# Kernel tuning notes

Hardware: AMD Instinct MI355X
Metric: run time of the kernel (lower is better)

Reference implementation:

```python
import jax, jax.numpy as jnp
import numpy as np

N = 2048
D_MODEL = 1024
N_HEADS = 16
D_HEAD = D_MODEL // N_HEADS


def setup_inputs() -> dict:
    key = jax.random.key(0)
    ks = jax.random.split(key, 12)
    s = 1.0 / np.sqrt(D_MODEL)
    inp = {
        "x": jax.random.normal(ks[0], (N, D_MODEL), dtype=jnp.float32),
        "edge_bias": jax.random.normal(ks[1], (N, N, N_HEADS), dtype=jnp.float32) * 0.1,
        # torch.nn.Linear convention: y = x @ W.T + b, W: [out, in]
        "Wq": jax.random.normal(ks[2], (D_MODEL, D_MODEL), dtype=jnp.float32) * s,
        "bq": jax.random.normal(ks[3], (D_MODEL,), dtype=jnp.float32) * s,
        "Wk": jax.random.normal(ks[4], (D_MODEL, D_MODEL), dtype=jnp.float32) * s,
        "bk": jax.random.normal(ks[5], (D_MODEL,), dtype=jnp.float32) * s,
        "Wv": jax.random.normal(ks[6], (D_MODEL, D_MODEL), dtype=jnp.float32) * s,
        "bv": jax.random.normal(ks[7], (D_MODEL,), dtype=jnp.float32) * s,
        "Wo": jax.random.normal(ks[8], (D_MODEL, D_MODEL), dtype=jnp.float32) * s,
        "bo": jax.random.normal(ks[9], (D_MODEL,), dtype=jnp.float32) * s,
    }
    return inp


def reference(x, edge_bias, Wq, bq, Wk, bk, Wv, bv, Wo, bo):
    # x: [N, d], edge_bias: [N, N, H]
    scale = D_HEAD ** -0.5
    q = (x @ Wq.T + bq).reshape(N, N_HEADS, D_HEAD)  # [N, H, Dh]
    k = (x @ Wk.T + bk).reshape(N, N_HEADS, D_HEAD)
    v = (x @ Wv.T + bv).reshape(N, N_HEADS, D_HEAD)
    # attn[h, i, j] = q_i . k_j * scale + edge_bias[i, j, h]
    attn = jnp.einsum("nhd,mhd->hnm", q, k) * scale
    attn = attn + jnp.transpose(edge_bias, (2, 0, 1))
    attn = jax.nn.softmax(attn, axis=-1)
    # dropout is identity in eval/reference mode
    out = jnp.einsum("hnm,mhd->nhd", attn, v).reshape(N, D_MODEL)
    return out @ Wo.T + bo
```

## Files before the change

### kernel.cpp

```cpp
#include <hip/hip_runtime.h>
#include <math.h>

#define NTOK 2048
#define DM   1024
#define NH   16
#define DH   64
#define GM   2048
#define GN   1024
#define GK   1024
#define SCALE 0.125f

typedef __attribute__((ext_vector_type(8))) short short8;
typedef __attribute__((ext_vector_type(4))) float floatx4;
typedef unsigned short ushort_t;

__device__ __forceinline__ unsigned short f2bf(float f) {
    unsigned u = __builtin_bit_cast(unsigned, f);
    u += 0x7fffu + ((u >> 16) & 1u);
    return (unsigned short)(u >> 16);
}

__global__ __launch_bounds__(256) void convert5(
    const float* __restrict__ x,  const float* __restrict__ wq,
    const float* __restrict__ wk, const float* __restrict__ wv,
    const float* __restrict__ wo, ushort_t* __restrict__ dst)
{
    const size_t i4 = (size_t)blockIdx.x * 256 + threadIdx.x;
    const float* src; size_t off;
    if      (i4 <  524288) { src = x;  off = 0;       }
    else if (i4 <  786432) { src = wq; off = 524288;  }
    else if (i4 < 1048576) { src = wk; off = 786432;  }
    else if (i4 < 1310720) { src = wv; off = 1048576; }
    else                   { src = wo; off = 1310720; }
    float4 v = ((const float4*)src)[i4 - off];
    ushort4 o;
    o.x = f2bf(v.x); o.y = f2bf(v.y); o.z = f2bf(v.z); o.w = f2bf(v.w);
    ((ushort4*)dst)[i4] = o;
}

template<int BM, int BN>
__global__ __launch_bounds__(256) void gemm_bt(
    const ushort_t* __restrict__ A,
    const ushort_t* __restrict__ B0, const ushort_t* __restrict__ B1,
    const ushort_t* __restrict__ B2,
    const float* __restrict__ bi0, const float* __restrict__ bi1,
    const float* __restrict__ bi2,
    void* C0, void* C1, void* C2, int mode0, int mode1, int mode2)
{
    constexpr int AC = BM * 4 / 256;
    constexpr int BC = BN * 4 / 256;
    constexpr int FI = BM / 32;
    constexpr int FJ = BN / 32;
    constexpr int WM = BM / 2;
    constexpr int WN = BN / 2;

    const int z = blockIdx.z;
    const ushort_t* B   = (z == 0) ? B0  : (z == 1) ? B1  : B2;
    const float*    bia = (z == 0) ? bi0 : (z == 1) ? bi1 : bi2;
    void*           C   = (z == 0) ? C0  : (z == 1) ? C1  : C2;
    const int mode      = (z == 0) ? mode0 : (z == 1) ? mode1 : mode2;

    __shared__ __align__(16) ushort_t As[BM][32];
    __shared__ __align__(16) ushort_t Bs[BN][32];

    const int t    = threadIdx.x;
    const int w    = t >> 6;
    const int L    = t & 63;
    const int r16  = L & 15;
    const int quad = L >> 4;
    const int wm   = w & 1;
    const int wn   = w >> 1;

    const int m0 = blockIdx.y * BM;
    const int n0 = blockIdx.x * BN;

    const int srow = t >> 2;
    const int skc  = (t & 3) * 8;

    const ushort_t* ap = A + (size_t)(m0 + srow) * GK + skc;
    const ushort_t* bp = B + (size_t)(n0 + srow) * GK + skc;

    floatx4 acc[FI][FJ];
#pragma unroll
    for (int i = 0; i < FI; ++i)
#pragma unroll
        for (int j = 0; j < FJ; ++j) acc[i][j] = (floatx4){0.f, 0.f, 0.f, 0.f};

    short8 areg[AC], breg[BC];
#pragma unroll
    for (int c = 0; c < AC; ++c) areg[c] = *(const short8*)(ap + (size_t)c * 64 * GK);
#pragma unroll
    for (int c = 0; c < BC; ++c) breg[c] = *(const short8*)(bp + (size_t)c * 64 * GK);

    for (int ks = 0; ks < GK / 32; ++ks) {
        __syncthreads();
#pragma unroll
        for (int c = 0; c < AC; ++c) *(short8*)&As[c * 64 + srow][skc] = areg[c];
#pragma unroll
        for (int c = 0; c < BC; ++c) *(short8*)&Bs[c * 64 + srow][skc] = breg[c];
        __syncthreads();
        if (ks < GK / 32 - 1) {
            ap += 32; bp += 32;
#pragma unroll
            for (int c = 0; c < AC; ++c) areg[c] = *(const short8*)(ap + (size_t)c * 64 * GK);
#pragma unroll
            for (int c = 0; c < BC; ++c) breg[c] = *(const short8*)(bp + (size_t)c * 64 * GK);
        }
        short8 af[FI], bf[FJ];
#pragma unroll
        for (int fi = 0; fi < FI; ++fi)
            af[fi] = *(const short8*)&As[wm * WM + fi * 16 + r16][quad * 8];
#pragma unroll
        for (int fj = 0; fj < FJ; ++fj)
            bf[fj] = *(const short8*)&Bs[wn * WN + fj * 16 + r16][quad * 8];
#pragma unroll
        for (int fi = 0; fi < FI; ++fi)
#pragma unroll
            for (int fj = 0; fj < FJ; ++fj)
                acc[fi][fj] = __builtin_amdgcn_mfma_f32_16x16x32_bf16(
                    af[fi], bf[fj], acc[fi][fj], 0, 0, 0);
    }

#pragma unroll
    for (int fj = 0; fj < FJ; ++fj) {
        const int col = n0 + wn * WN + fj * 16 + r16;
        const float bv = bia[col];
#pragma unroll
        for (int fi = 0; fi < FI; ++fi) {
            const int row0 = m0 + wm * WM + fi * 16 + 4 * quad;
            floatx4 c = acc[fi][fj];
            if (mode == 2) {
                float* Cf = (float*)C;
#pragma unroll
                for (int i = 0; i < 4; ++i)
                    Cf[(size_t)(row0 + i) * GN + col] = c[i] + bv;
            } else if (mode == 0) {
                ushort_t* Cb = (ushort_t*)C;
#pragma unroll
                for (int i = 0; i < 4; ++i)
                    Cb[(size_t)(row0 + i) * GN + col] = f2bf(c[i] + bv);
            } else {
                ushort_t* Cb = (ushort_t*)C;
                ushort4 pk;
                pk.x = f2bf(c[0] + bv); pk.y = f2bf(c[1] + bv);
                pk.z = f2bf(c[2] + bv); pk.w = f2bf(c[3] + bv);
                *(ushort4*)(Cb + (size_t)col * GM + row0) = pk;
            }
        }
    }
}

#define NT   (NTOK / 32)
#define NCH  4
#define NTCH (NT / NCH)
#define JCH  (NTOK / NCH)

__global__ __launch_bounds__(256) void attn2(
    const ushort_t* __restrict__ q, const ushort_t* __restrict__ k,
    const ushort_t* __restrict__ vT, const float* __restrict__ bias,
    float* __restrict__ opart, float* __restrict__ lpart)
{
    __shared__ float    Bb[2][4][16][33];
    __shared__ ushort_t Ps[4][16][40];

    const int b    = blockIdx.x;
    const int ch   = blockIdx.y;
    const int jb   = ch * JCH;
    const int hg   = (b >> 3) & 3;
    const int it   = (b & 7) | ((b >> 5) << 3);
    const int i0   = it * 16;
    const int t    = threadIdx.x;
    const int w    = t >> 6;
    const int L    = t & 63;
    const int r16  = L & 15;
    const int quad = L >> 4;
    const int h    = hg * 4 + w;

#define kAddr(J0, JH, KC) (k  + (size_t)((J0) + (JH)*16 + r16) * DM + h*DH + (KC)*32 + quad*8)
#define vAddr(J0, DB)     (vT + (size_t)(h*DH + (DB)*16 + r16) * NTOK + (J0) + quad*8)
#define bAddr(J0, CI)     (bias + ((size_t)(i0 + (CI)*8 + (t>>5)) * NTOK + (J0) + (t&31)) * NH + hg*4)

    short8 qf[2];
#pragma unroll
    for (int kc = 0; kc < 2; ++kc)
        qf[kc] = *(const short8*)(q + (size_t)(i0 + r16) * DM + h * DH + kc * 32 + quad * 8);

    short8 kf[2][4];
    short8 vf[2][4];
    float4 bst[2];

    kf[0][0] = *(const short8*)kAddr(jb, 0, 0);
    kf[0][1] = *(const short8*)kAddr(jb, 0, 1);
    kf[0][2] = *(const short8*)kAddr(jb, 1, 0);
    kf[0][3] = *(const short8*)kAddr(jb, 1, 1);
    vf[0][0] = *(const short8*)vAddr(jb, 0);
    vf[0][1] = *(const short8*)vAddr(jb, 1);
    vf[0][2] = *(const short8*)vAddr(jb, 2);
    vf[0][3] = *(const short8*)vAddr(jb, 3);
    bst[0] = *(const float4*)bAddr(jb, 0);
    bst[1] = *(const float4*)bAddr(jb, 1);
    Bb[0][0][0 + (t >> 5)][t & 31] = bst[0].x;
    Bb[0][1][0 + (t >> 5)][t & 31] = bst[0].y;
    Bb[0][2][0 + (t >> 5)][t & 31] = bst[0].z;
    Bb[0][3][0 + (t >> 5)][t & 31] = bst[0].w;
    Bb[0][0][8 + (t >> 5)][t & 31] = bst[1].x;
    Bb[0][1][8 + (t >> 5)][t & 31] = bst[1].y;
    Bb[0][2][8 + (t >> 5)][t & 31] = bst[1].z;
    Bb[0][3][8 + (t >> 5)][t & 31] = bst[1].w;
    __syncthreads();

    floatx4 o[4];
#pragma unroll
    for (int d = 0; d < 4; ++d) o[d] = (floatx4){0.f, 0.f, 0.f, 0.f};
    float lrow[4] = {0.f, 0.f, 0.f, 0.f};

#define TILE(JT, CUR, NXT)                                                      \
  {                                                                             \
    const bool pre = (JT) < NTCH - 1;                                           \
    const int j0n = jb + ((JT) + 1) * 32;                                       \
    if (pre) {                                                                  \
      kf[NXT][0] = *(const short8*)kAddr(j0n, 0, 0);                            \
      kf[NXT][1] = *(const short8*)kAddr(j0n, 0, 1);                            \
      kf[NXT][2] = *(const short8*)kAddr(j0n, 1, 0);                            \
      kf[NXT][3] = *(const short8*)kAddr(j0n, 1, 1);                            \
      vf[NXT][0] = *(const short8*)vAddr(j0n, 0);                               \
      vf[NXT][1] = *(const short8*)vAddr(j0n, 1);                               \
      vf[NXT][2] = *(const short8*)vAddr(j0n, 2);                               \
      vf[NXT][3] = *(const short8*)vAddr(j0n, 3);                               \
      bst[0] = *(const float4*)bAddr(j0n, 0);                                   \
      bst[1] = *(const float4*)bAddr(j0n, 1);                                   \
    }                                                                           \
    floatx4 s0 = (floatx4){0.f, 0.f, 0.f, 0.f};                                 \
    floatx4 s1 = (floatx4){0.f, 0.f, 0.f, 0.f};                                 \
    s0 = __builtin_amdgcn_mfma_f32_16x16x32_bf16(qf[0], kf[CUR][0], s0, 0,0,0); \
    s0 = __builtin_amdgcn_mfma_f32_16x16x32_bf16(qf[1], kf[CUR][1], s0, 0,0,0); \
    s1 = __builtin_amdgcn_mfma_f32_16x16x32_bf16(qf[0], kf[CUR][2], s1, 0,0,0); \
    s1 = __builtin_amdgcn_mfma_f32_16x16x32_bf16(qf[1], kf[CUR][3], s1, 0,0,0); \
    _Pragma("unroll")                                                           \
    for (int ii = 0; ii < 4; ++ii) {                                            \
      const float bv0 = Bb[CUR][w][4 * quad + ii][r16];                         \
      const float bv1 = Bb[CUR][w][4 * quad + ii][16 + r16];                    \
      const float p0 = __expf(fmaf(s0[ii], SCALE, bv0));                        \
      const float p1 = __expf(fmaf(s1[ii], SCALE, bv1));                        \
      lrow[ii] += p0 + p1;                                                      \
      Ps[w][4 * quad + ii][r16]      = f2bf(p0);                                \
      Ps[w][4 * quad + ii][16 + r16] = f2bf(p1);                                \
    }                                                                           \
    short8 pf = *(const short8*)&Ps[w][r16][quad * 8];                          \
    o[0] = __builtin_amdgcn_mfma_f32_16x16x32_bf16(pf, vf[CUR][0], o[0], 0,0,0);\
    o[1] = __builtin_amdgcn_mfma_f32_16x16x32_bf16(pf, vf[CUR][1], o[1], 0,0,0);\
    o[2] = __builtin_amdgcn_mfma_f32_16x16x32_bf16(pf, vf[CUR][2], o[2], 0,0,0);\
    o[3] = __builtin_amdgcn_mfma_f32_16x16x32_bf16(pf, vf[CUR][3], o[3], 0,0,0);\
    if (pre) {                                                                  \
      Bb[NXT][0][0 + (t >> 5)][t & 31] = bst[0].x;                              \
      Bb[NXT][1][0 + (t >> 5)][t & 31] = bst[0].y;                              \
      Bb[NXT][2][0 + (t >> 5)][t & 31] = bst[0].z;                              \
      Bb[NXT][3][0 + (t >> 5)][t & 31] = bst[0].w;                              \
      Bb[NXT][0][8 + (t >> 5)][t & 31] = bst[1].x;                              \
      Bb[NXT][1][8 + (t >> 5)][t & 31] = bst[1].y;                              \
      Bb[NXT][2][8 + (t >> 5)][t & 31] = bst[1].z;                              \
      Bb[NXT][3][8 + (t >> 5)][t & 31] = bst[1].w;                              \
    }                                                                           \
    __syncthreads();                                                            \
  }

    for (int jt = 0; jt < NTCH; jt += 2) {
        TILE(jt, 0, 1)
        TILE(jt + 1, 1, 0)
    }

    float lred[4];
#pragma unroll
    for (int ii = 0; ii < 4; ++ii) {
        float s = lrow[ii];
#pragma unroll
        for (int d = 1; d < 16; d <<= 1) s += __shfl_xor(s, d);
        lred[ii] = s;
    }
    if (r16 == 0) {
#pragma unroll
        for (int ii = 0; ii < 4; ++ii)
            lpart[(size_t)ch * NH * NTOK + (size_t)h * NTOK + i0 + 4 * quad + ii] = lred[ii];
    }

    float* op = opart + (size_t)ch * NTOK * DM;
#pragma unroll
    for (int db = 0; db < 4; ++db)
#pragma unroll
        for (int ii = 0; ii < 4; ++ii)
            op[(size_t)(i0 + 4 * quad + ii) * DM + h * DH + db * 16 + r16] = o[db][ii];
#undef TILE
#undef kAddr
#undef vAddr
#undef bAddr
}

__global__ __launch_bounds__(256) void attn_fin(
    const float* __restrict__ opart, const float* __restrict__ lpart,
    ushort_t* __restrict__ ao)
{
    const int idx = blockIdx.x * 256 + threadIdx.x;
    const int n   = idx >> 8;
    const int d4  = idx & 255;
    const int h   = d4 >> 4;
    const size_t base = (size_t)n * DM + (size_t)d4 * 4;
    float4 s = {0.f, 0.f, 0.f, 0.f};
    float  l = 0.f;
#pragma unroll
    for (int c = 0; c < NCH; ++c) {
        float4 p = *(const float4*)(opart + (size_t)c * NTOK * DM + base);
        s.x += p.x; s.y += p.y; s.z += p.z; s.w += p.w;
        l += lpart[(size_t)c * NH * NTOK + (size_t)h * NTOK + n];
    }
    const float inv = 1.f / l;
    ushort4 o;
    o.x = f2bf(s.x * inv); o.y = f2bf(s.y * inv);
    o.z = f2bf(s.z * inv); o.w = f2bf(s.w * inv);
    ((ushort4*)ao)[idx] = o;
}

extern "C" void kernel_launch(void* const* d_in, const int* in_sizes, int n_in,
                              void* d_out, int out_size, void* d_ws, size_t ws_size,
                              hipStream_t stream)
{
    const float* x  = (const float*)d_in[0];
    const float* eb = (const float*)d_in[1];
    const float* Wq = (const float*)d_in[2];
    const float* bq = (const float*)d_in[3];
    const float* Wk = (const float*)d_in[4];
    const float* bk = (const float*)d_in[5];
    const float* Wv = (const float*)d_in[6];
    const float* bv = (const float*)d_in[7];
    const float* Wo = (const float*)d_in[8];
    const float* bo = (const float*)d_in[9];
    float* out = (float*)d_out;
    (void)in_sizes; (void)n_in; (void)out_size; (void)ws_size;

    const size_t E1 = (size_t)1024 * 1024;
    ushort_t* wsb = (ushort_t*)d_ws;
    ushort_t* xb  = wsb;
    ushort_t* Wqb = wsb + 2 * E1;
    ushort_t* Wkb = wsb + 3 * E1;
    ushort_t* Wvb = wsb + 4 * E1;
    ushort_t* Wob = wsb + 5 * E1;
    ushort_t* qb  = wsb + 6 * E1;
    ushort_t* kb  = wsb + 8 * E1;
    ushort_t* vTb = wsb + 10 * E1;
    ushort_t* aob = wsb + 12 * E1;
    float* opart = (float*)(wsb + 14 * E1);
    float* lpart = opart + (size_t)NCH * NTOK * DM;

    convert5<<<6144, 256, 0, stream>>>(x, Wq, Wk, Wv, Wo, wsb);

    {
        dim3 grid(GN / 64, GM / 128, 3);
        gemm_bt<128, 64><<<grid, 256, 0, stream>>>(
            xb, Wqb, Wkb, Wvb, bq, bk, bv,
            qb, kb, vTb, 0, 0, 1);
    }
    {
        dim3 grid(512, NCH, 1);
        attn2<<<grid, 256, 0, stream>>>(qb, kb, vTb, eb, opart, lpart);
    }
    attn_fin<<<NTOK * DM / 4 / 256, 256, 0, stream>>>(opart, lpart, aob);

    {
        dim3 grid(GN / 64, GM / 64, 1);
        gemm_bt<64, 64><<<grid, 256, 0, stream>>>(
            aob, Wob, Wob, Wob, bo, bo, bo,
            out, out, out, 2, 2, 2);
    }
}
```

Measured before the change: 528.9 us.

## Process all heads per attention block to coalesce edge-bias loads

```diff
diff --git a/kernel.cpp b/kernel.cpp
--- a/kernel.cpp
+++ b/kernel.cpp
@@ -155,30 +155,32 @@
 #define NTCH (NT / NCH)
 #define JCH  (NTOK / NCH)
 
-__global__ __launch_bounds__(256) void attn2(
+__global__ __launch_bounds__(1024) void attn3(
     const ushort_t* __restrict__ q, const ushort_t* __restrict__ k,
     const ushort_t* __restrict__ vT, const float* __restrict__ bias,
     float* __restrict__ opart, float* __restrict__ lpart)
 {
-    __shared__ float    Bb[2][4][16][33];
-    __shared__ ushort_t Ps[4][16][40];
-
-    const int b    = blockIdx.x;
+    __shared__ float    Bb[2][16][16][33];
+    __shared__ ushort_t Ps[16][16][40];
+
+    const int it   = blockIdx.x;
     const int ch   = blockIdx.y;
     const int jb   = ch * JCH;
-    const int hg   = (b >> 3) & 3;
-    const int it   = (b & 7) | ((b >> 5) << 3);
     const int i0   = it * 16;
     const int t    = threadIdx.x;
     const int w    = t >> 6;
     const int L    = t & 63;
     const int r16  = L & 15;
     const int quad = L >> 4;
-    const int h    = hg * 4 + w;
+    const int h    = w;
+
+    const int si = t >> 6;
+    const int sj = (L >> 1);
+    const int sh = (L & 1) * 8;
 
 #define kAddr(J0, JH, KC) (k  + (size_t)((J0) + (JH)*16 + r16) * DM + h*DH + (KC)*32 + quad*8)
 #define vAddr(J0, DB)     (vT + (size_t)(h*DH + (DB)*16 + r16) * NTOK + (J0) + quad*8)
-#define bAddr(J0, CI)     (bias + ((size_t)(i0 + (CI)*8 + (t>>5)) * NTOK + (J0) + (t&31)) * NH + hg*4)
+#define bAddr(J0)         (bias + ((size_t)(i0 + si) * NTOK + (J0) + sj) * NH + sh)
 
     short8 qf[2];
 #pragma unroll
@@ -197,16 +199,16 @@
     vf[0][1] = *(const short8*)vAddr(jb, 1);
     vf[0][2] = *(const short8*)vAddr(jb, 2);
     vf[0][3] = *(const short8*)vAddr(jb, 3);
-    bst[0] = *(const float4*)bAddr(jb, 0);
-    bst[1] = *(const float4*)bAddr(jb, 1);
-    Bb[0][0][0 + (t >> 5)][t & 31] = bst[0].x;
-    Bb[0][1][0 + (t >> 5)][t & 31] = bst[0].y;
-    Bb[0][2][0 + (t >> 5)][t & 31] = bst[0].z;
-    Bb[0][3][0 + (t >> 5)][t & 31] = bst[0].w;
-    Bb[0][0][8 + (t >> 5)][t & 31] = bst[1].x;
-    Bb[0][1][8 + (t >> 5)][t & 31] = bst[1].y;
-    Bb[0][2][8 + (t >> 5)][t & 31] = bst[1].z;
-    Bb[0][3][8 + (t >> 5)][t & 31] = bst[1].w;
+    bst[0] = *(const float4*)bAddr(jb);
+    bst[1] = *(const float4*)(bAddr(jb) + 4);
+    Bb[0][sh + 0][si][sj] = bst[0].x;
+    Bb[0][sh + 1][si][sj] = bst[0].y;
+    Bb[0][sh + 2][si][sj] = bst[0].z;
+    Bb[0][sh + 3][si][sj] = bst[0].w;
+    Bb[0][sh + 4][si][sj] = bst[1].x;
+    Bb[0][sh + 5][si][sj] = bst[1].y;
+    Bb[0][sh + 6][si][sj] = bst[1].z;
+    Bb[0][sh + 7][si][sj] = bst[1].w;
     __syncthreads();
 
     floatx4 o[4];
@@ -227,8 +229,8 @@
       vf[NXT][1] = *(const short8*)vAddr(j0n, 1);                               \
       vf[NXT][2] = *(const short8*)vAddr(j0n, 2);                               \
       vf[NXT][3] = *(const short8*)vAddr(j0n, 3);                               \
-      bst[0] = *(const float4*)bAddr(j0n, 0);                                   \
-      bst[1] = *(const float4*)bAddr(j0n, 1);                                   \
+      bst[0] = *(const float4*)bAddr(j0n);                                      \
+      bst[1] = *(const float4*)(bAddr(j0n) + 4);                                \
     }                                                                           \
     floatx4 s0 = (floatx4){0.f, 0.f, 0.f, 0.f};                                 \
     floatx4 s1 = (floatx4){0.f, 0.f, 0.f, 0.f};                                 \
@@ -252,14 +254,14 @@
     o[2] = __builtin_amdgcn_mfma_f32_16x16x32_bf16(pf, vf[CUR][2], o[2], 0,0,0);\
     o[3] = __builtin_amdgcn_mfma_f32_16x16x32_bf16(pf, vf[CUR][3], o[3], 0,0,0);\
     if (pre) {                                                                  \
-      Bb[NXT][0][0 + (t >> 5)][t & 31] = bst[0].x;                              \
-      Bb[NXT][1][0 + (t >> 5)][t & 31] = bst[0].y;                              \
-      Bb[NXT][2][0 + (t >> 5)][t & 31] = bst[0].z;                              \
-      Bb[NXT][3][0 + (t >> 5)][t & 31] = bst[0].w;                              \
-      Bb[NXT][0][8 + (t >> 5)][t & 31] = bst[1].x;                              \
-      Bb[NXT][1][8 + (t >> 5)][t & 31] = bst[1].y;                              \
-      Bb[NXT][2][8 + (t >> 5)][t & 31] = bst[1].z;                              \
-      Bb[NXT][3][8 + (t >> 5)][t & 31] = bst[1].w;                              \
+      Bb[NXT][sh + 0][si][sj] = bst[0].x;                                       \
+      Bb[NXT][sh + 1][si][sj] = bst[0].y;                                       \
+      Bb[NXT][sh + 2][si][sj] = bst[0].z;                                       \
+      Bb[NXT][sh + 3][si][sj] = bst[0].w;                                       \
+      Bb[NXT][sh + 4][si][sj] = bst[1].x;                                       \
+      Bb[NXT][sh + 5][si][sj] = bst[1].y;                                       \
+      Bb[NXT][sh + 6][si][sj] = bst[1].z;                                       \
+      Bb[NXT][sh + 7][si][sj] = bst[1].w;                                       \
     }                                                                           \
     __syncthreads();                                                            \
   }
@@ -359,8 +361,8 @@
             qb, kb, vTb, 0, 0, 1);
     }
     {
-        dim3 grid(512, NCH, 1);
-        attn2<<<grid, 256, 0, stream>>>(qb, kb, vTb, eb, opart, lpart);
+        dim3 grid(NTOK / 16, NCH, 1);
+        attn3<<<grid, 1024, 0, stream>>>(qb, kb, vTb, eb, opart, lpart);
     }
     attn_fin<<<NTOK * DM / 4 / 256, 256, 0, stream>>>(opart, lpart, aob);
 
```

New measurement: 560.4 us. 6.0% more time.

## Process 32 query rows per attention block to reuse K/V fragments

Applied to the files above, without the earlier changes.

```diff
diff --git a/kernel.cpp b/kernel.cpp
--- a/kernel.cpp
+++ b/kernel.cpp
@@ -154,13 +154,14 @@
 #define NCH  4
 #define NTCH (NT / NCH)
 #define JCH  (NTOK / NCH)
-
-__global__ __launch_bounds__(256) void attn2(
+#define IB   32
+
+__global__ __launch_bounds__(256) void attn4(
     const ushort_t* __restrict__ q, const ushort_t* __restrict__ k,
     const ushort_t* __restrict__ vT, const float* __restrict__ bias,
     float* __restrict__ opart, float* __restrict__ lpart)
 {
-    __shared__ float    Bb[2][4][16][33];
+    __shared__ float    Bb[2][4][IB][33];
     __shared__ ushort_t Ps[4][16][40];
 
     const int b    = blockIdx.x;
@@ -168,7 +169,7 @@
     const int jb   = ch * JCH;
     const int hg   = (b >> 3) & 3;
     const int it   = (b & 7) | ((b >> 5) << 3);
-    const int i0   = it * 16;
+    const int i0   = it * IB;
     const int t    = threadIdx.x;
     const int w    = t >> 6;
     const int L    = t & 63;
@@ -180,15 +181,22 @@
 #define vAddr(J0, DB)     (vT + (size_t)(h*DH + (DB)*16 + r16) * NTOK + (J0) + quad*8)
 #define bAddr(J0, CI)     (bias + ((size_t)(i0 + (CI)*8 + (t>>5)) * NTOK + (J0) + (t&31)) * NH + hg*4)
 
-    short8 qf[2];
-#pragma unroll
-    for (int kc = 0; kc < 2; ++kc)
-        qf[kc] = *(const short8*)(q + (size_t)(i0 + r16) * DM + h * DH + kc * 32 + quad * 8);
+    short8 qf[2][2];
+#pragma unroll
+    for (int r = 0; r < 2; ++r)
+#pragma unroll
+        for (int kc = 0; kc < 2; ++kc)
+            qf[r][kc] = *(const short8*)(q + (size_t)(i0 + r * 16 + r16) * DM
+                                           + h * DH + kc * 32 + quad * 8);
 
     short8 kf[2][4];
     short8 vf[2][4];
-    float4 bst[2];
-
+    float4 bst[4];
+
+    bst[0] = *(const float4*)bAddr(jb, 0);
+    bst[1] = *(const float4*)bAddr(jb, 1);
+    bst[2] = *(const float4*)bAddr(jb, 2);
+    bst[3] = *(const float4*)bAddr(jb, 3);
     kf[0][0] = *(const short8*)kAddr(jb, 0, 0);
     kf[0][1] = *(const short8*)kAddr(jb, 0, 1);
     kf[0][2] = *(const short8*)kAddr(jb, 1, 0);
@@ -197,28 +205,31 @@
     vf[0][1] = *(const short8*)vAddr(jb, 1);
     vf[0][2] = *(const short8*)vAddr(jb, 2);
     vf[0][3] = *(const short8*)vAddr(jb, 3);
-    bst[0] = *(const float4*)bAddr(jb, 0);
-    bst[1] = *(const float4*)bAddr(jb, 1);
-    Bb[0][0][0 + (t >> 5)][t & 31] = bst[0].x;
-    Bb[0][1][0 + (t >> 5)][t & 31] = bst[0].y;
-    Bb[0][2][0 + (t >> 5)][t & 31] = bst[0].z;
-    Bb[0][3][0 + (t >> 5)][t & 31] = bst[0].w;
-    Bb[0][0][8 + (t >> 5)][t & 31] = bst[1].x;
-    Bb[0][1][8 + (t >> 5)][t & 31] = bst[1].y;
-    Bb[0][2][8 + (t >> 5)][t & 31] = bst[1].z;
-    Bb[0][3][8 + (t >> 5)][t & 31] = bst[1].w;
+#pragma unroll
+    for (int ci = 0; ci < 4; ++ci) {
+        Bb[0][0][ci * 8 + (t >> 5)][t & 31] = bst[ci].x;
+        Bb[0][1][ci * 8 + (t >> 5)][t & 31] = bst[ci].y;
+        Bb[0][2][ci * 8 + (t >> 5)][t & 31] = bst[ci].z;
+        Bb[0][3][ci * 8 + (t >> 5)][t & 31] = bst[ci].w;
+    }
     __syncthreads();
 
-    floatx4 o[4];
-#pragma unroll
-    for (int d = 0; d < 4; ++d) o[d] = (floatx4){0.f, 0.f, 0.f, 0.f};
-    float lrow[4] = {0.f, 0.f, 0.f, 0.f};
+    floatx4 o[2][4];
+#pragma unroll
+    for (int r = 0; r < 2; ++r)
+#pragma unroll
+        for (int d = 0; d < 4; ++d) o[r][d] = (floatx4){0.f, 0.f, 0.f, 0.f};
+    float lrow[2][4] = {{0.f,0.f,0.f,0.f},{0.f,0.f,0.f,0.f}};
 
 #define TILE(JT, CUR, NXT)                                                      \
   {                                                                             \
     const bool pre = (JT) < NTCH - 1;                                           \
     const int j0n = jb + ((JT) + 1) * 32;                                       \
     if (pre) {                                                                  \
+      bst[0] = *(const float4*)bAddr(j0n, 0);                                   \
+      bst[1] = *(const float4*)bAddr(j0n, 1);                                   \
+      bst[2] = *(const float4*)bAddr(j0n, 2);                                   \
+      bst[3] = *(const float4*)bAddr(j0n, 3);                                   \
       kf[NXT][0] = *(const short8*)kAddr(j0n, 0, 0);                            \
       kf[NXT][1] = *(const short8*)kAddr(j0n, 0, 1);                            \
       kf[NXT][2] = *(const short8*)kAddr(j0n, 1, 0);                            \
@@ -227,39 +238,61 @@
       vf[NXT][1] = *(const short8*)vAddr(j0n, 1);                               \
       vf[NXT][2] = *(const short8*)vAddr(j0n, 2);                               \
       vf[NXT][3] = *(const short8*)vAddr(j0n, 3);                               \
-      bst[0] = *(const float4*)bAddr(j0n, 0);                                   \
-      bst[1] = *(const float4*)bAddr(j0n, 1);                                   \
-    }                                                                           \
-    floatx4 s0 = (floatx4){0.f, 0.f, 0.f, 0.f};                                 \
-    floatx4 s1 = (floatx4){0.f, 0.f, 0.f, 0.f};                                 \
-    s0 = __builtin_amdgcn_mfma_f32_16x16x32_bf16(qf[0], kf[CUR][0], s0, 0,0,0); \
-    s0 = __builtin_amdgcn_mfma_f32_16x16x32_bf16(qf[1], kf[CUR][1], s0, 0,0,0); \
-    s1 = __builtin_amdgcn_mfma_f32_16x16x32_bf16(qf[0], kf[CUR][2], s1, 0,0,0); \
-    s1 = __builtin_amdgcn_mfma_f32_16x16x32_bf16(qf[1], kf[CUR][3], s1, 0,0,0); \
+    }                                                                           \
+    floatx4 s00 = (floatx4){0.f,0.f,0.f,0.f};                                   \
+    floatx4 s01 = (floatx4){0.f,0.f,0.f,0.f};                                   \
+    floatx4 s10 = (floatx4){0.f,0.f,0.f,0.f};                                   \
+    floatx4 s11 = (floatx4){0.f,0.f,0.f,0.f};                                   \
+    s00 = __builtin_amdgcn_mfma_f32_16x16x32_bf16(qf[0][0], kf[CUR][0], s00, 0,0,0); \
+    s00 = __builtin_amdgcn_mfma_f32_16x16x32_bf16(qf[0][1], kf[CUR][1], s00, 0,0,0); \
+    s01 = __builtin_amdgcn_mfma_f32_16x16x32_bf16(qf[0][0], kf[CUR][2], s01, 0,0,0); \
+    s01 = __builtin_amdgcn_mfma_f32_16x16x32_bf16(qf[0][1], kf[CUR][3], s01, 0,0,0); \
+    s10 = __builtin_amdgcn_mfma_f32_16x16x32_bf16(qf[1][0], kf[CUR][0], s10, 0,0,0); \
+    s10 = __builtin_amdgcn_mfma_f32_16x16x32_bf16(qf[1][1], kf[CUR][1], s10, 0,0,0); \
+    s11 = __builtin_amdgcn_mfma_f32_16x16x32_bf16(qf[1][0], kf[CUR][2], s11, 0,0,0); \
+    s11 = __builtin_amdgcn_mfma_f32_16x16x32_bf16(qf[1][1], kf[CUR][3], s11, 0,0,0); \
     _Pragma("unroll")                                                           \
     for (int ii = 0; ii < 4; ++ii) {                                            \
       const float bv0 = Bb[CUR][w][4 * quad + ii][r16];                         \
       const float bv1 = Bb[CUR][w][4 * quad + ii][16 + r16];                    \
-      const float p0 = __expf(fmaf(s0[ii], SCALE, bv0));                        \
-      const float p1 = __expf(fmaf(s1[ii], SCALE, bv1));                        \
-      lrow[ii] += p0 + p1;                                                      \
+      const float p0 = __expf(fmaf(s00[ii], SCALE, bv0));                       \
+      const float p1 = __expf(fmaf(s01[ii], SCALE, bv1));                       \
+      lrow[0][ii] += p0 + p1;                                                   \
       Ps[w][4 * quad + ii][r16]      = f2bf(p0);                                \
       Ps[w][4 * quad + ii][16 + r16] = f2bf(p1);                                \
     }                                                                           \
-    short8 pf = *(const short8*)&Ps[w][r16][quad * 8];                          \
-    o[0] = __builtin_amdgcn_mfma_f32_16x16x32_bf16(pf, vf[CUR][0], o[0], 0,0,0);\
-    o[1] = __builtin_amdgcn_mfma_f32_16x16x32_bf16(pf, vf[CUR][1], o[1], 0,0,0);\
-    o[2] = __builtin_amdgcn_mfma_f32_16x16x32_bf16(pf, vf[CUR][2], o[2], 0,0,0);\
-    o[3] = __builtin_amdgcn_mfma_f32_16x16x32_bf16(pf, vf[CUR][3], o[3], 0,0,0);\
+    {                                                                           \
+      short8 pf = *(const short8*)&Ps[w][r16][quad * 8];                        \
+      o[0][0] = __builtin_amdgcn_mfma_f32_16x16x32_bf16(pf, vf[CUR][0], o[0][0], 0,0,0); \
+      o[0][1] = __builtin_amdgcn_mfma_f32_16x16x32_bf16(pf, vf[CUR][1], o[0][1], 0,0,0); \
+      o[0][2] = __builtin_amdgcn_mfma_f32_16x16x32_bf16(pf, vf[CUR][2], o[0][2], 0,0,0); \
+      o[0][3] = __builtin_amdgcn_mfma_f32_16x16x32_bf16(pf, vf[CUR][3], o[0][3], 0,0,0); \
+    }                                                                           \
+    _Pragma("unroll")                                                           \
+    for (int ii = 0; ii < 4; ++ii) {                                            \
+      const float bv0 = Bb[CUR][w][16 + 4 * quad + ii][r16];                    \
+      const float bv1 = Bb[CUR][w][16 + 4 * quad + ii][16 + r16];               \
+      const float p0 = __expf(fmaf(s10[ii], SCALE, bv0));                       \
+      const float p1 = __expf(fmaf(s11[ii], SCALE, bv1));                       \
+      lrow[1][ii] += p0 + p1;                                                   \
+      Ps[w][4 * quad + ii][r16]      = f2bf(p0);                                \
+      Ps[w][4 * quad + ii][16 + r16] = f2bf(p1);                                \
+    }                                                                           \
+    {                                                                           \
+      short8 pf = *(const short8*)&Ps[w][r16][quad * 8];                        \
+      o[1][0] = __builtin_amdgcn_mfma_f32_16x16x32_bf16(pf, vf[CUR][0], o[1][0], 0,0,0); \
+      o[1][1] = __builtin_amdgcn_mfma_f32_16x16x32_bf16(pf, vf[CUR][1], o[1][1], 0,0,0); \
+      o[1][2] = __builtin_amdgcn_mfma_f32_16x16x32_bf16(pf, vf[CUR][2], o[1][2], 0,0,0); \
+      o[1][3] = __builtin_amdgcn_mfma_f32_16x16x32_bf16(pf, vf[CUR][3], o[1][3], 0,0,0); \
+    }                                                                           \
     if (pre) {                                                                  \
-      Bb[NXT][0][0 + (t >> 5)][t & 31] = bst[0].x;                              \
-      Bb[NXT][1][0 + (t >> 5)][t & 31] = bst[0].y;                              \
-      Bb[NXT][2][0 + (t >> 5)][t & 31] = bst[0].z;                              \
-      Bb[NXT][3][0 + (t >> 5)][t & 31] = bst[0].w;                              \
-      Bb[NXT][0][8 + (t >> 5)][t & 31] = bst[1].x;                              \
-      Bb[NXT][1][8 + (t >> 5)][t & 31] = bst[1].y;                              \
-      Bb[NXT][2][8 + (t >> 5)][t & 31] = bst[1].z;                              \
-      Bb[NXT][3][8 + (t >> 5)][t & 31] = bst[1].w;                              \
+      _Pragma("unroll")                                                         \
+      for (int ci = 0; ci < 4; ++ci) {                                          \
+        Bb[NXT][0][ci * 8 + (t >> 5)][t & 31] = bst[ci].x;                      \
+        Bb[NXT][1][ci * 8 + (t >> 5)][t & 31] = bst[ci].y;                      \
+        Bb[NXT][2][ci * 8 + (t >> 5)][t & 31] = bst[ci].z;                      \
+        Bb[NXT][3][ci * 8 + (t >> 5)][t & 31] = bst[ci].w;                      \
+      }                                                                         \
     }                                                                           \
     __syncthreads();                                                            \
   }
@@ -269,26 +302,33 @@
         TILE(jt + 1, 1, 0)
     }
 
-    float lred[4];
-#pragma unroll
-    for (int ii = 0; ii < 4; ++ii) {
-        float s = lrow[ii];
-#pragma unroll
-        for (int d = 1; d < 16; d <<= 1) s += __shfl_xor(s, d);
-        lred[ii] = s;
-    }
-    if (r16 == 0) {
-#pragma unroll
-        for (int ii = 0; ii < 4; ++ii)
-            lpart[(size_t)ch * NH * NTOK + (size_t)h * NTOK + i0 + 4 * quad + ii] = lred[ii];
+#pragma unroll
+    for (int r = 0; r < 2; ++r) {
+        float lred[4];
+#pragma unroll
+        for (int ii = 0; ii < 4; ++ii) {
+            float s = lrow[r][ii];
+#pragma unroll
+            for (int d = 1; d < 16; d <<= 1) s += __shfl_xor(s, d);
+            lred[ii] = s;
+        }
+        if (r16 == 0) {
+#pragma unroll
+            for (int ii = 0; ii < 4; ++ii)
+                lpart[(size_t)ch * NH * NTOK + (size_t)h * NTOK
+                      + i0 + r * 16 + 4 * quad + ii] = lred[ii];
+        }
     }
 
     float* op = opart + (size_t)ch * NTOK * DM;
 #pragma unroll
-    for (int db = 0; db < 4; ++db)
-#pragma unroll
-        for (int ii = 0; ii < 4; ++ii)
-            op[(size_t)(i0 + 4 * quad + ii) * DM + h * DH + db * 16 + r16] = o[db][ii];
+    for (int r = 0; r < 2; ++r)
+#pragma unroll
+        for (int db = 0; db < 4; ++db)
+#pragma unroll
+            for (int ii = 0; ii < 4; ++ii)
+                op[(size_t)(i0 + r * 16 + 4 * quad + ii) * DM
+                   + h * DH + db * 16 + r16] = o[r][db][ii];
 #undef TILE
 #undef kAddr
 #undef vAddr
@@ -359,8 +399,8 @@
             qb, kb, vTb, 0, 0, 1);
     }
     {
-        dim3 grid(512, NCH, 1);
-        attn2<<<grid, 256, 0, stream>>>(qb, kb, vTb, eb, opart, lpart);
+        dim3 grid((NTOK / IB) * 4, NCH, 1);
+        attn4<<<grid, 256, 0, stream>>>(qb, kb, vTb, eb, opart, lpart);
     }
     attn_fin<<<NTOK * DM / 4 / 256, 256, 0, stream>>>(opart, lpart, aob);
 
```

Measured after the change: 496.3 us. 1.07x faster.
